# Performance work log

Hardware: AMD Instinct MI355X
Metric: run time of the kernel (lower is better)

Reference implementation:

```python
import jax, jax.numpy as jnp
import numpy as np

N_NODES = 50000
N_EDGES = 800000
NODE_DIM = 16
EDGE_DIM = 16
HIDDEN = 128
OUT_DIM = 4
N_BLOCKS = 3  # len(layers) - 1


def setup_inputs() -> dict:
    key = jax.random.key(0)
    ks = jax.random.split(key, 12)
    s = 0.05
    x = jax.random.normal(ks[0], (N_NODES, NODE_DIM), dtype=jnp.float32)
    edge_index = jax.random.randint(ks[1], (2, N_EDGES), 0, N_NODES, dtype=jnp.int64)
    edge_attr = jax.random.normal(ks[2], (N_EDGES, EDGE_DIM), dtype=jnp.float32)
    lift_w = jax.random.normal(ks[3], (NODE_DIM, HIDDEN), dtype=jnp.float32) * s
    lift_b = jnp.zeros((HIDDEN,), dtype=jnp.float32)
    # Stacked per-block params: root linear on x_i, message linear on [x_j || e_ij]
    root_w = jax.random.normal(ks[4], (N_BLOCKS, HIDDEN, HIDDEN), dtype=jnp.float32) * s
    root_b = jnp.zeros((N_BLOCKS, HIDDEN), dtype=jnp.float32)
    msg_w = jax.random.normal(ks[5], (N_BLOCKS, HIDDEN + EDGE_DIM, HIDDEN), dtype=jnp.float32) * s
    msg_b = jnp.zeros((N_BLOCKS, HIDDEN), dtype=jnp.float32)
    proj_w = jax.random.normal(ks[6], (HIDDEN, OUT_DIM), dtype=jnp.float32) * s
    proj_b = jnp.zeros((OUT_DIM,), dtype=jnp.float32)
    return {
        "x": x, "edge_index": edge_index, "edge_attr": edge_attr,
        "lift_w": lift_w, "lift_b": lift_b,
        "root_w": root_w, "root_b": root_b,
        "msg_w": msg_w, "msg_b": msg_b,
        "proj_w": proj_w, "proj_b": proj_b,
    }


def reference(x, edge_index, edge_attr, lift_w, lift_b, root_w, root_b, msg_w, msg_b, proj_w, proj_b):
    src = edge_index[0]  # message source j
    dst = edge_index[1]  # message target i
    n = x.shape[0]
    h = x @ lift_w + lift_b  # lift: [N, H]
    n_blocks = root_w.shape[0]
    for i in range(n_blocks):  # small fixed loop over layers
        m_in = jnp.concatenate([h[src], edge_attr], axis=-1)  # [E, H+Ed]
        msg = m_in @ msg_w[i] + msg_b[i]                       # [E, H]
        agg = jax.ops.segment_sum(msg, dst, num_segments=n)    # scatter-add [N, H]
        out = h @ root_w[i] + root_b[i] + agg + h               # conv + identity skip
        # last block runs with use_activation=False
        h = jax.nn.gelu(out) if i < n_blocks - 1 else out
    return h @ proj_w + proj_b  # projection [N, OUT_DIM]
```

## Files before the change

### kernel.cpp

```cpp
#include <hip/hip_runtime.h>

#define NN 50000
#define NE 800000
#define ND 16
#define ED 16
#define H  128
#define OD 4
#define KPK 288
#define LDAK 296
#define SLOT 64

#define LIFT_B (NN * H / 256)
#define PACK_B (3 * 128 * KPK / 256)
#define ZERO_B ((NN + 255) / 256)

typedef __bf16 bf16;
typedef __attribute__((ext_vector_type(8))) __bf16 bf16x8;
typedef __attribute__((ext_vector_type(4))) float f32x4;

static __device__ __forceinline__ float bf2f(unsigned short u) {
  return __builtin_bit_cast(float, (unsigned int)u << 16);
}
static __device__ __forceinline__ unsigned short f2bfu(float f) {
  return __builtin_bit_cast(unsigned short, (bf16)f);
}
static __device__ __forceinline__ unsigned int pk2(float a, float b) {
  return (unsigned int)f2bfu(a) | ((unsigned int)f2bfu(b) << 16);
}

__global__ __launch_bounds__(256) void prologue_kernel(
    const float* __restrict__ x, const float* __restrict__ lw,
    const float* __restrict__ lb, bf16* __restrict__ h,
    const float* __restrict__ msg_w, const float* __restrict__ root_w,
    const float* __restrict__ root_b, const float* __restrict__ msg_b,
    bf16* __restrict__ Wp, int* __restrict__ cursor) {
  int bid = blockIdx.x;
  if (bid < LIFT_B) {
    int idx = bid * 256 + threadIdx.x;
    int n = idx >> 7, k = idx & 127;
    float acc = lb[k];
    const float* xr = x + (size_t)n * ND;
#pragma unroll
    for (int j = 0; j < ND; ++j) acc = fmaf(xr[j], lw[j * H + k], acc);
    h[idx] = (bf16)acc;
  } else if (bid < LIFT_B + PACK_B) {
    int idx = (bid - LIFT_B) * 256 + threadIdx.x;
    int b = idx / (128 * KPK);
    int r = idx % (128 * KPK);
    int c = r / KPK, k = r % KPK;
    float v = 0.f;
    if (k < 128)       v = root_w[((size_t)b * 128 + k) * 128 + c];
    else if (k < 256)  v = msg_w[((size_t)b * 144 + (k - 128)) * 128 + c];
    else if (k < 272)  v = msg_w[((size_t)b * 144 + 128 + (k - 256)) * 128 + c];
    else if (k == 272) v = msg_b[(size_t)b * 128 + c];
    else if (k == 273) v = root_b[(size_t)b * 128 + c];
    Wp[idx] = (bf16)v;
  } else {
    int i = (bid - LIFT_B - PACK_B) * 256 + threadIdx.x;
    if (i < NN) cursor[i] = 0;
  }
}

__global__ __launch_bounds__(256) void csr_fill_kernel(
    const int* __restrict__ ei, int* __restrict__ cursor,
    int2* __restrict__ csr) {
  int part = blockIdx.x & 7;
  int e0 = (blockIdx.x >> 3) * 1024 + threadIdx.x * 4;
  if (e0 >= NE) return;
  int4 s4 = *(const int4*)&ei[e0];
  int4 d4 = *(const int4*)&ei[NE + e0];
#pragma unroll
  for (int j = 0; j < 4; ++j) {
    int dst = (&d4.x)[j];
    if ((int)(((long long)dst * 8) / NN) == part) {
      int pos = atomicAdd(&cursor[dst], 1);
      if (pos < SLOT)
        csr[dst * SLOT + pos] = make_int2((&s4.x)[j], e0 + j);
    }
  }
}

__global__ __launch_bounds__(256) void gather_ea_kernel(
    const int* __restrict__ cursor, const int2* __restrict__ csr,
    const bf16* __restrict__ h, const float* __restrict__ ea,
    bf16* __restrict__ hagg, bf16* __restrict__ stat) {
  int t = threadIdx.x;
  int node = blockIdx.x * 16 + (t >> 4);
  int li = t & 15;
  int k8 = li * 8;
  int deg = cursor[node];
  int s = node * SLOT, e = s + deg;
  const int* ci = (const int*)csr;
  const unsigned short* Hu = (const unsigned short*)h;

  float acc[8];
#pragma unroll
  for (int j = 0; j < 8; ++j) acc[j] = 0.f;
  float aea = 0.f;

  int p = s;
  for (; p + 4 <= e; p += 4) {
    int s0 = ci[2 * p],     e0 = ci[2 * p + 1];
    int s1 = ci[2 * p + 2], e1 = ci[2 * p + 3];
    int s2 = ci[2 * p + 4], e2 = ci[2 * p + 5];
    int s3 = ci[2 * p + 6], e3 = ci[2 * p + 7];
    uint4 v0 = *(const uint4*)&Hu[(size_t)s0 * H + k8];
    uint4 v1 = *(const uint4*)&Hu[(size_t)s1 * H + k8];
    uint4 v2 = *(const uint4*)&Hu[(size_t)s2 * H + k8];
    uint4 v3 = *(const uint4*)&Hu[(size_t)s3 * H + k8];
    float a0 = ea[(size_t)e0 * ED + li];
    float a1 = ea[(size_t)e1 * ED + li];
    float a2 = ea[(size_t)e2 * ED + li];
    float a3 = ea[(size_t)e3 * ED + li];
#pragma unroll
    for (int j = 0; j < 4; ++j) {
      unsigned int w0 = (&v0.x)[j], w1 = (&v1.x)[j], w2 = (&v2.x)[j], w3 = (&v3.x)[j];
      acc[2 * j]     += (bf2f((unsigned short)(w0 & 0xffff)) + bf2f((unsigned short)(w1 & 0xffff)))
                      + (bf2f((unsigned short)(w2 & 0xffff)) + bf2f((unsigned short)(w3 & 0xffff)));
      acc[2 * j + 1] += (bf2f((unsigned short)(w0 >> 16)) + bf2f((unsigned short)(w1 >> 16)))
                      + (bf2f((unsigned short)(w2 >> 16)) + bf2f((unsigned short)(w3 >> 16)));
    }
    aea += (a0 + a1) + (a2 + a3);
  }
  for (; p < e; ++p) {
    int s0 = ci[2 * p], e0 = ci[2 * p + 1];
    uint4 v0 = *(const uint4*)&Hu[(size_t)s0 * H + k8];
    aea += ea[(size_t)e0 * ED + li];
#pragma unroll
    for (int j = 0; j < 4; ++j) {
      unsigned int w0 = (&v0.x)[j];
      acc[2 * j]     += bf2f((unsigned short)(w0 & 0xffff));
      acc[2 * j + 1] += bf2f((unsigned short)(w0 >> 16));
    }
  }

  uint4 o;
  o.x = pk2(acc[0], acc[1]);
  o.y = pk2(acc[2], acc[3]);
  o.z = pk2(acc[4], acc[5]);
  o.w = pk2(acc[6], acc[7]);
  *(uint4*)&((unsigned short*)hagg)[(size_t)node * H + k8] = o;

  unsigned short* S = (unsigned short*)stat;
  S[(size_t)node * 32 + li] = f2bfu(aea);
  float v2 = (li == 0) ? (float)deg : (li == 1 ? 1.0f : 0.0f);
  S[(size_t)node * 32 + 16 + li] = f2bfu(v2);
}

__global__ __launch_bounds__(256) void gather_h_kernel(
    const int* __restrict__ cursor, const int2* __restrict__ csr,
    const bf16* __restrict__ h, bf16* __restrict__ hagg) {
  int t = threadIdx.x;
  int node = blockIdx.x * 16 + (t >> 4);
  int li = t & 15;
  int k8 = li * 8;
  int deg = cursor[node];
  int s = node * SLOT, e = s + deg;
  const int* ci = (const int*)csr;
  const unsigned short* Hu = (const unsigned short*)h;

  float acc[8];
#pragma unroll
  for (int j = 0; j < 8; ++j) acc[j] = 0.f;

  int p = s;
  for (; p + 4 <= e; p += 4) {
    int s0 = ci[2 * p];
    int s1 = ci[2 * p + 2];
    int s2 = ci[2 * p + 4];
    int s3 = ci[2 * p + 6];
    uint4 v0 = *(const uint4*)&Hu[(size_t)s0 * H + k8];
    uint4 v1 = *(const uint4*)&Hu[(size_t)s1 * H + k8];
    uint4 v2 = *(const uint4*)&Hu[(size_t)s2 * H + k8];
    uint4 v3 = *(const uint4*)&Hu[(size_t)s3 * H + k8];
#pragma unroll
    for (int j = 0; j < 4; ++j) {
      unsigned int w0 = (&v0.x)[j], w1 = (&v1.x)[j], w2 = (&v2.x)[j], w3 = (&v3.x)[j];
      acc[2 * j]     += (bf2f((unsigned short)(w0 & 0xffff)) + bf2f((unsigned short)(w1 & 0xffff)))
                      + (bf2f((unsigned short)(w2 & 0xffff)) + bf2f((unsigned short)(w3 & 0xffff)));
      acc[2 * j + 1] += (bf2f((unsigned short)(w0 >> 16)) + bf2f((unsigned short)(w1 >> 16)))
                      + (bf2f((unsigned short)(w2 >> 16)) + bf2f((unsigned short)(w3 >> 16)));
    }
  }
  for (; p < e; ++p) {
    int s0 = ci[2 * p];
    uint4 v0 = *(const uint4*)&Hu[(size_t)s0 * H + k8];
#pragma unroll
    for (int j = 0; j < 4; ++j) {
      unsigned int w0 = (&v0.x)[j];
      acc[2 * j]     += bf2f((unsigned short)(w0 & 0xffff));
      acc[2 * j + 1] += bf2f((unsigned short)(w0 >> 16));
    }
  }

  uint4 o;
  o.x = pk2(acc[0], acc[1]);
  o.y = pk2(acc[2], acc[3]);
  o.z = pk2(acc[4], acc[5]);
  o.w = pk2(acc[6], acc[7]);
  *(uint4*)&((unsigned short*)hagg)[(size_t)node * H + k8] = o;
}

__global__ __launch_bounds__(256, 3) void gemm_mfma_kernel(
    bf16* __restrict__ h, const bf16* __restrict__ hagg,
    const bf16* __restrict__ stat, const bf16* __restrict__ Wp,
    const float* __restrict__ pw, const float* __restrict__ pb,
    float* __restrict__ out, int act) {
  __shared__ bf16 as[64 * LDAK];
  int t = threadIdx.x;
  int lane = t & 63;
  int wv = t >> 6;
  int l15 = lane & 15, g = lane >> 4;
  int c0w = wv * 32;

  bf16x8 bq[9][2];
#pragma unroll
  for (int kk = 0; kk < 9; ++kk)
#pragma unroll
    for (int ni = 0; ni < 2; ++ni)
      bq[kk][ni] = *(const bf16x8*)(Wp + (size_t)(c0w + ni * 16 + l15) * KPK + kk * 32 + g * 8);

  int m0 = blockIdx.x * 64;
#pragma unroll
  for (int i = 0; i < 9; ++i) {
    int idx = i * 256 + t;
    int r = idx / 36, seg = idx % 36;
    int node = m0 + r;
    float4 v = make_float4(0.f, 0.f, 0.f, 0.f);
    if (node < NN) {
      const bf16* src;
      if (seg < 16)      src = h    + (size_t)node * H + seg * 8;
      else if (seg < 32) src = hagg + (size_t)node * H + (seg - 16) * 8;
      else               src = stat + (size_t)node * 32 + (seg - 32) * 8;
      v = *(const float4*)src;
    }
    *(float4*)(as + r * LDAK + seg * 8) = v;
  }
  __syncthreads();

  f32x4 acc[4][2];
#pragma unroll
  for (int mi = 0; mi < 4; ++mi)
#pragma unroll
    for (int ni = 0; ni < 2; ++ni)
      acc[mi][ni] = (f32x4){0.f, 0.f, 0.f, 0.f};

#pragma unroll
  for (int kk = 0; kk < 9; ++kk) {
    bf16x8 af[4];
#pragma unroll
    for (int mi = 0; mi < 4; ++mi)
      af[mi] = *(const bf16x8*)(as + (mi * 16 + l15) * LDAK + kk * 32 + g * 8);
#pragma unroll
    for (int mi = 0; mi < 4; ++mi)
#pragma unroll
      for (int ni = 0; ni < 2; ++ni)
        acc[mi][ni] = __builtin_amdgcn_mfma_f32_16x16x32_bf16(
            af[mi], bq[kk][ni], acc[mi][ni], 0, 0, 0);
  }

  if (act) {
#pragma unroll
    for (int mi = 0; mi < 4; ++mi) {
#pragma unroll
      for (int ni = 0; ni < 2; ++ni) {
#pragma unroll
        for (int i = 0; i < 4; ++i) {
          int rloc = mi * 16 + g * 4 + i;
          int row = m0 + rloc;
          int col = c0w + ni * 16 + l15;
          if (row < NN) {
            float v = acc[mi][ni][i];
            v += bf2f(__builtin_bit_cast(unsigned short, as[rloc * LDAK + col]));
            float u = 0.7978845608028654f * (v + 0.044715f * v * v * v);
            v = 0.5f * v * (1.f + tanhf(u));
            h[(size_t)row * H + col] = (bf16)v;
          }
        }
      }
    }
  } else {
    __syncthreads();
#pragma unroll
    for (int mi = 0; mi < 4; ++mi) {
#pragma unroll
      for (int ni = 0; ni < 2; ++ni) {
#pragma unroll
        for (int i = 0; i < 4; ++i) {
          int rloc = mi * 16 + g * 4 + i;
          int col = c0w + ni * 16 + l15;
          float v = acc[mi][ni][i];
          v += bf2f(__builtin_bit_cast(unsigned short, as[rloc * LDAK + col]));
          as[rloc * LDAK + col] = (bf16)v;
        }
      }
    }
    __syncthreads();
    int row = t >> 2, o = t & 3;
    float accp = pb[o];
    const unsigned short* hr = (const unsigned short*)(as + row * LDAK);
#pragma unroll
    for (int j = 0; j < H; ++j)
      accp = fmaf(bf2f(hr[j]), pw[j * OD + o], accp);
    if (m0 + row < NN) out[(size_t)(m0 + row) * OD + o] = accp;
  }
}

extern "C" void kernel_launch(void* const* d_in, const int* in_sizes, int n_in,
                              void* d_out, int out_size, void* d_ws, size_t ws_size,
                              hipStream_t stream) {
  const float* x       = (const float*)d_in[0];
  const int*   ei      = (const int*)d_in[1];
  const float* ea      = (const float*)d_in[2];
  const float* lift_w  = (const float*)d_in[3];
  const float* lift_b  = (const float*)d_in[4];
  const float* root_w  = (const float*)d_in[5];
  const float* root_b  = (const float*)d_in[6];
  const float* msg_w   = (const float*)d_in[7];
  const float* msg_b   = (const float*)d_in[8];
  const float* proj_w  = (const float*)d_in[9];
  const float* proj_b  = (const float*)d_in[10];
  float* out = (float*)d_out;

  char* w = (char*)d_ws;
  bf16*  h      = (bf16*)w;              w += (size_t)NN * H * 2;
  bf16*  hagg   = (bf16*)w;              w += (size_t)NN * H * 2;
  bf16*  stat   = (bf16*)w;              w += (size_t)NN * 32 * 2;
  bf16*  Wp     = (bf16*)w;              w += (size_t)3 * 128 * KPK * 2;
  int2*  csr    = (int2*)w;              w += (size_t)NN * SLOT * 8;
  int*   cursor  = (int*)w;

  prologue_kernel<<<LIFT_B + PACK_B + ZERO_B, 256, 0, stream>>>(
      x, lift_w, lift_b, h, msg_w, root_w, root_b, msg_b, Wp, cursor);
  csr_fill_kernel<<<8 * ((NE + 1023) / 1024), 256, 0, stream>>>(ei, cursor, csr);

  for (int b = 0; b < 3; ++b) {
    if (b == 0)
      gather_ea_kernel<<<NN / 16, 256, 0, stream>>>(cursor, csr, h, ea, hagg, stat);
    else
      gather_h_kernel<<<NN / 16, 256, 0, stream>>>(cursor, csr, h, hagg);
    gemm_mfma_kernel<<<(NN + 63) / 64, 256, 0, stream>>>(
        h, hagg, stat, Wp + (size_t)b * 128 * KPK,
        proj_w, proj_b, out, b < 2 ? 1 : 0);
  }
}
```

Baseline: 247.2 us.

## Fuse neighbor gather into MFMA GEMM kernel with ping-pong h buffers

```diff
diff --git a/kernel.cpp b/kernel.cpp
--- a/kernel.cpp
+++ b/kernel.cpp
@@ -80,138 +80,22 @@
   }
 }
 
-__global__ __launch_bounds__(256) void gather_ea_kernel(
+__global__ __launch_bounds__(256, 3) void fused_kernel(
+    const bf16* __restrict__ hin, bf16* __restrict__ hout,
     const int* __restrict__ cursor, const int2* __restrict__ csr,
-    const bf16* __restrict__ h, const float* __restrict__ ea,
-    bf16* __restrict__ hagg, bf16* __restrict__ stat) {
-  int t = threadIdx.x;
-  int node = blockIdx.x * 16 + (t >> 4);
-  int li = t & 15;
-  int k8 = li * 8;
-  int deg = cursor[node];
-  int s = node * SLOT, e = s + deg;
-  const int* ci = (const int*)csr;
-  const unsigned short* Hu = (const unsigned short*)h;
-
-  float acc[8];
-#pragma unroll
-  for (int j = 0; j < 8; ++j) acc[j] = 0.f;
-  float aea = 0.f;
-
-  int p = s;
-  for (; p + 4 <= e; p += 4) {
-    int s0 = ci[2 * p],     e0 = ci[2 * p + 1];
-    int s1 = ci[2 * p + 2], e1 = ci[2 * p + 3];
-    int s2 = ci[2 * p + 4], e2 = ci[2 * p + 5];
-    int s3 = ci[2 * p + 6], e3 = ci[2 * p + 7];
-    uint4 v0 = *(const uint4*)&Hu[(size_t)s0 * H + k8];
-    uint4 v1 = *(const uint4*)&Hu[(size_t)s1 * H + k8];
-    uint4 v2 = *(const uint4*)&Hu[(size_t)s2 * H + k8];
-    uint4 v3 = *(const uint4*)&Hu[(size_t)s3 * H + k8];
-    float a0 = ea[(size_t)e0 * ED + li];
-    float a1 = ea[(size_t)e1 * ED + li];
-    float a2 = ea[(size_t)e2 * ED + li];
-    float a3 = ea[(size_t)e3 * ED + li];
-#pragma unroll
-    for (int j = 0; j < 4; ++j) {
-      unsigned int w0 = (&v0.x)[j], w1 = (&v1.x)[j], w2 = (&v2.x)[j], w3 = (&v3.x)[j];
-      acc[2 * j]     += (bf2f((unsigned short)(w0 & 0xffff)) + bf2f((unsigned short)(w1 & 0xffff)))
-                      + (bf2f((unsigned short)(w2 & 0xffff)) + bf2f((unsigned short)(w3 & 0xffff)));
-      acc[2 * j + 1] += (bf2f((unsigned short)(w0 >> 16)) + bf2f((unsigned short)(w1 >> 16)))
-                      + (bf2f((unsigned short)(w2 >> 16)) + bf2f((unsigned short)(w3 >> 16)));
-    }
-    aea += (a0 + a1) + (a2 + a3);
-  }
-  for (; p < e; ++p) {
-    int s0 = ci[2 * p], e0 = ci[2 * p + 1];
-    uint4 v0 = *(const uint4*)&Hu[(size_t)s0 * H + k8];
-    aea += ea[(size_t)e0 * ED + li];
-#pragma unroll
-    for (int j = 0; j < 4; ++j) {
-      unsigned int w0 = (&v0.x)[j];
-      acc[2 * j]     += bf2f((unsigned short)(w0 & 0xffff));
-      acc[2 * j + 1] += bf2f((unsigned short)(w0 >> 16));
-    }
-  }
-
-  uint4 o;
-  o.x = pk2(acc[0], acc[1]);
-  o.y = pk2(acc[2], acc[3]);
-  o.z = pk2(acc[4], acc[5]);
-  o.w = pk2(acc[6], acc[7]);
-  *(uint4*)&((unsigned short*)hagg)[(size_t)node * H + k8] = o;
-
-  unsigned short* S = (unsigned short*)stat;
-  S[(size_t)node * 32 + li] = f2bfu(aea);
-  float v2 = (li == 0) ? (float)deg : (li == 1 ? 1.0f : 0.0f);
-  S[(size_t)node * 32 + 16 + li] = f2bfu(v2);
-}
-
-__global__ __launch_bounds__(256) void gather_h_kernel(
-    const int* __restrict__ cursor, const int2* __restrict__ csr,
-    const bf16* __restrict__ h, bf16* __restrict__ hagg) {
-  int t = threadIdx.x;
-  int node = blockIdx.x * 16 + (t >> 4);
-  int li = t & 15;
-  int k8 = li * 8;
-  int deg = cursor[node];
-  int s = node * SLOT, e = s + deg;
-  const int* ci = (const int*)csr;
-  const unsigned short* Hu = (const unsigned short*)h;
-
-  float acc[8];
-#pragma unroll
-  for (int j = 0; j < 8; ++j) acc[j] = 0.f;
-
-  int p = s;
-  for (; p + 4 <= e; p += 4) {
-    int s0 = ci[2 * p];
-    int s1 = ci[2 * p + 2];
-    int s2 = ci[2 * p + 4];
-    int s3 = ci[2 * p + 6];
-    uint4 v0 = *(const uint4*)&Hu[(size_t)s0 * H + k8];
-    uint4 v1 = *(const uint4*)&Hu[(size_t)s1 * H + k8];
-    uint4 v2 = *(const uint4*)&Hu[(size_t)s2 * H + k8];
-    uint4 v3 = *(const uint4*)&Hu[(size_t)s3 * H + k8];
-#pragma unroll
-    for (int j = 0; j < 4; ++j) {
-      unsigned int w0 = (&v0.x)[j], w1 = (&v1.x)[j], w2 = (&v2.x)[j], w3 = (&v3.x)[j];
-      acc[2 * j]     += (bf2f((unsigned short)(w0 & 0xffff)) + bf2f((unsigned short)(w1 & 0xffff)))
-                      + (bf2f((unsigned short)(w2 & 0xffff)) + bf2f((unsigned short)(w3 & 0xffff)));
-      acc[2 * j + 1] += (bf2f((unsigned short)(w0 >> 16)) + bf2f((unsigned short)(w1 >> 16)))
-                      + (bf2f((unsigned short)(w2 >> 16)) + bf2f((unsigned short)(w3 >> 16)));
-    }
-  }
-  for (; p < e; ++p) {
-    int s0 = ci[2 * p];
-    uint4 v0 = *(const uint4*)&Hu[(size_t)s0 * H + k8];
-#pragma unroll
-    for (int j = 0; j < 4; ++j) {
-      unsigned int w0 = (&v0.x)[j];
-      acc[2 * j]     += bf2f((unsigned short)(w0 & 0xffff));
-      acc[2 * j + 1] += bf2f((unsigned short)(w0 >> 16));
-    }
-  }
-
-  uint4 o;
-  o.x = pk2(acc[0], acc[1]);
-  o.y = pk2(acc[2], acc[3]);
-  o.z = pk2(acc[4], acc[5]);
-  o.w = pk2(acc[6], acc[7]);
-  *(uint4*)&((unsigned short*)hagg)[(size_t)node * H + k8] = o;
-}
-
-__global__ __launch_bounds__(256, 3) void gemm_mfma_kernel(
-    bf16* __restrict__ h, const bf16* __restrict__ hagg,
-    const bf16* __restrict__ stat, const bf16* __restrict__ Wp,
-    const float* __restrict__ pw, const float* __restrict__ pb,
-    float* __restrict__ out, int act) {
+    const float* __restrict__ ea, bf16* __restrict__ stat,
+    const bf16* __restrict__ Wp, const float* __restrict__ pw,
+    const float* __restrict__ pb, float* __restrict__ out,
+    int iter, int act) {
   __shared__ bf16 as[64 * LDAK];
   int t = threadIdx.x;
   int lane = t & 63;
   int wv = t >> 6;
   int l15 = lane & 15, g = lane >> 4;
   int c0w = wv * 32;
+  int w16 = t >> 4;
+  int li = t & 15;
+  int m0 = blockIdx.x * 64;
 
   bf16x8 bq[9][2];
 #pragma unroll
@@ -220,21 +104,120 @@
     for (int ni = 0; ni < 2; ++ni)
       bq[kk][ni] = *(const bf16x8*)(Wp + (size_t)(c0w + ni * 16 + l15) * KPK + kk * 32 + g * 8);
 
-  int m0 = blockIdx.x * 64;
-#pragma unroll
-  for (int i = 0; i < 9; ++i) {
-    int idx = i * 256 + t;
-    int r = idx / 36, seg = idx % 36;
-    int node = m0 + r;
-    float4 v = make_float4(0.f, 0.f, 0.f, 0.f);
-    if (node < NN) {
-      const bf16* src;
-      if (seg < 16)      src = h    + (size_t)node * H + seg * 8;
-      else if (seg < 32) src = hagg + (size_t)node * H + (seg - 16) * 8;
-      else               src = stat + (size_t)node * 32 + (seg - 32) * 8;
-      v = *(const float4*)src;
-    }
-    *(float4*)(as + r * LDAK + seg * 8) = v;
+  const unsigned short* Hu = (const unsigned short*)hin;
+  const unsigned short* S = (const unsigned short*)stat;
+  const int* ci = (const int*)csr;
+  int k8 = li * 8;
+
+  for (int q = 0; q < 4; ++q) {
+    int nloc = q * 16 + w16;
+    int node = m0 + nloc;
+    bool valid = node < NN;
+    int deg = valid ? cursor[node] : 0;
+    int s = node * SLOT, e = s + deg;
+
+    uint4 hv = make_uint4(0u, 0u, 0u, 0u);
+    if (valid) hv = *(const uint4*)&Hu[(size_t)node * H + k8];
+    *(uint4*)(as + nloc * LDAK + k8) = hv;
+
+    float acc[8];
+#pragma unroll
+    for (int j = 0; j < 8; ++j) acc[j] = 0.f;
+    float aea = 0.f;
+
+    int p = s;
+    if (iter == 0) {
+      for (; p + 4 <= e; p += 4) {
+        int s0 = ci[2 * p],     e0 = ci[2 * p + 1];
+        int s1 = ci[2 * p + 2], e1 = ci[2 * p + 3];
+        int s2 = ci[2 * p + 4], e2 = ci[2 * p + 5];
+        int s3 = ci[2 * p + 6], e3 = ci[2 * p + 7];
+        uint4 v0 = *(const uint4*)&Hu[(size_t)s0 * H + k8];
+        uint4 v1 = *(const uint4*)&Hu[(size_t)s1 * H + k8];
+        uint4 v2 = *(const uint4*)&Hu[(size_t)s2 * H + k8];
+        uint4 v3 = *(const uint4*)&Hu[(size_t)s3 * H + k8];
+        float a0 = ea[(size_t)e0 * ED + li];
+        float a1 = ea[(size_t)e1 * ED + li];
+        float a2 = ea[(size_t)e2 * ED + li];
+        float a3 = ea[(size_t)e3 * ED + li];
+#pragma unroll
+        for (int j = 0; j < 4; ++j) {
+          unsigned int w0 = (&v0.x)[j], w1 = (&v1.x)[j], w2 = (&v2.x)[j], w3 = (&v3.x)[j];
+          acc[2 * j]     += (bf2f((unsigned short)(w0 & 0xffff)) + bf2f((unsigned short)(w1 & 0xffff)))
+                          + (bf2f((unsigned short)(w2 & 0xffff)) + bf2f((unsigned short)(w3 & 0xffff)));
+          acc[2 * j + 1] += (bf2f((unsigned short)(w0 >> 16)) + bf2f((unsigned short)(w1 >> 16)))
+                          + (bf2f((unsigned short)(w2 >> 16)) + bf2f((unsigned short)(w3 >> 16)));
+        }
+        aea += (a0 + a1) + (a2 + a3);
+      }
+      for (; p < e; ++p) {
+        int s0 = ci[2 * p], e0 = ci[2 * p + 1];
+        uint4 v0 = *(const uint4*)&Hu[(size_t)s0 * H + k8];
+        aea += ea[(size_t)e0 * ED + li];
+#pragma unroll
+        for (int j = 0; j < 4; ++j) {
+          unsigned int w0 = (&v0.x)[j];
+          acc[2 * j]     += bf2f((unsigned short)(w0 & 0xffff));
+          acc[2 * j + 1] += bf2f((unsigned short)(w0 >> 16));
+        }
+      }
+    } else {
+      for (; p + 4 <= e; p += 4) {
+        int s0 = ci[2 * p];
+        int s1 = ci[2 * p + 2];
+        int s2 = ci[2 * p + 4];
+        int s3 = ci[2 * p + 6];
+        uint4 v0 = *(const uint4*)&Hu[(size_t)s0 * H + k8];
+        uint4 v1 = *(const uint4*)&Hu[(size_t)s1 * H + k8];
+        uint4 v2 = *(const uint4*)&Hu[(size_t)s2 * H + k8];
+        uint4 v3 = *(const uint4*)&Hu[(size_t)s3 * H + k8];
+#pragma unroll
+        for (int j = 0; j < 4; ++j) {
+          unsigned int w0 = (&v0.x)[j], w1 = (&v1.x)[j], w2 = (&v2.x)[j], w3 = (&v3.x)[j];
+          acc[2 * j]     += (bf2f((unsigned short)(w0 & 0xffff)) + bf2f((unsigned short)(w1 & 0xffff)))
+                          + (bf2f((unsigned short)(w2 & 0xffff)) + bf2f((unsigned short)(w3 & 0xffff)));
+          acc[2 * j + 1] += (bf2f((unsigned short)(w0 >> 16)) + bf2f((unsigned short)(w1 >> 16)))
+                          + (bf2f((unsigned short)(w2 >> 16)) + bf2f((unsigned short)(w3 >> 16)));
+        }
+      }
+      for (; p < e; ++p) {
+        int s0 = ci[2 * p];
+        uint4 v0 = *(const uint4*)&Hu[(size_t)s0 * H + k8];
+#pragma unroll
+        for (int j = 0; j < 4; ++j) {
+          unsigned int w0 = (&v0.x)[j];
+          acc[2 * j]     += bf2f((unsigned short)(w0 & 0xffff));
+          acc[2 * j + 1] += bf2f((unsigned short)(w0 >> 16));
+        }
+      }
+    }
+
+    uint4 o;
+    o.x = pk2(acc[0], acc[1]);
+    o.y = pk2(acc[2], acc[3]);
+    o.z = pk2(acc[4], acc[5]);
+    o.w = pk2(acc[6], acc[7]);
+    *(uint4*)(as + nloc * LDAK + 128 + k8) = o;
+
+    if (iter == 0) {
+      unsigned short sv0 = f2bfu(aea);
+      unsigned short sv1 = (li == 0) ? f2bfu((float)deg)
+                         : (li == 1) ? f2bfu(1.0f) : (unsigned short)0;
+      ((unsigned short*)as)[nloc * LDAK + 256 + li] = sv0;
+      ((unsigned short*)as)[nloc * LDAK + 272 + li] = sv1;
+      if (valid) {
+        ((unsigned short*)stat)[(size_t)node * 32 + li] = sv0;
+        ((unsigned short*)stat)[(size_t)node * 32 + 16 + li] = sv1;
+      }
+    } else {
+      unsigned short sv0 = 0, sv1 = 0;
+      if (valid) {
+        sv0 = S[(size_t)node * 32 + li];
+        sv1 = S[(size_t)node * 32 + 16 + li];
+      }
+      ((unsigned short*)as)[nloc * LDAK + 256 + li] = sv0;
+      ((unsigned short*)as)[nloc * LDAK + 272 + li] = sv1;
+    }
   }
   __syncthreads();
 
@@ -274,7 +257,7 @@
             v += bf2f(__builtin_bit_cast(unsigned short, as[rloc * LDAK + col]));
             float u = 0.7978845608028654f * (v + 0.044715f * v * v * v);
             v = 0.5f * v * (1.f + tanhf(u));
-            h[(size_t)row * H + col] = (bf16)v;
+            hout[(size_t)row * H + col] = (bf16)v;
           }
         }
       }
@@ -323,24 +306,23 @@
   float* out = (float*)d_out;
 
   char* w = (char*)d_ws;
-  bf16*  h      = (bf16*)w;              w += (size_t)NN * H * 2;
-  bf16*  hagg   = (bf16*)w;              w += (size_t)NN * H * 2;
+  bf16*  hA     = (bf16*)w;              w += (size_t)NN * H * 2;
+  bf16*  hB     = (bf16*)w;              w += (size_t)NN * H * 2;
   bf16*  stat   = (bf16*)w;              w += (size_t)NN * 32 * 2;
   bf16*  Wp     = (bf16*)w;              w += (size_t)3 * 128 * KPK * 2;
   int2*  csr    = (int2*)w;              w += (size_t)NN * SLOT * 8;
   int*   cursor  = (int*)w;
 
+  const int GB = (NN + 63) / 64;
+
   prologue_kernel<<<LIFT_B + PACK_B + ZERO_B, 256, 0, stream>>>(
-      x, lift_w, lift_b, h, msg_w, root_w, root_b, msg_b, Wp, cursor);
+      x, lift_w, lift_b, hA, msg_w, root_w, root_b, msg_b, Wp, cursor);
   csr_fill_kernel<<<8 * ((NE + 1023) / 1024), 256, 0, stream>>>(ei, cursor, csr);
 
-  for (int b = 0; b < 3; ++b) {
-    if (b == 0)
-      gather_ea_kernel<<<NN / 16, 256, 0, stream>>>(cursor, csr, h, ea, hagg, stat);
-    else
-      gather_h_kernel<<<NN / 16, 256, 0, stream>>>(cursor, csr, h, hagg);
-    gemm_mfma_kernel<<<(NN + 63) / 64, 256, 0, stream>>>(
-        h, hagg, stat, Wp + (size_t)b * 128 * KPK,
-        proj_w, proj_b, out, b < 2 ? 1 : 0);
-  }
-}
+  fused_kernel<<<GB, 256, 0, stream>>>(hA, hB, cursor, csr, ea, stat,
+                                       Wp, proj_w, proj_b, out, 0, 1);
+  fused_kernel<<<GB, 256, 0, stream>>>(hB, hA, cursor, csr, ea, stat,
+                                       Wp + (size_t)128 * KPK, proj_w, proj_b, out, 1, 1);
+  fused_kernel<<<GB, 256, 0, stream>>>(hA, hB, cursor, csr, ea, stat,
+                                       Wp + (size_t)2 * 128 * KPK, proj_w, proj_b, out, 2, 0);
+}
```

Result: slower. 304.3 us (+23.1%).
